# Kernel tuning notes

Measured on AMD Instinct MI355X. Metric: run time of the kernel, lower is better.

Reference implementation:

```python
import jax, jax.numpy as jnp
import numpy as np
from jax import lax

B, C, D, H, W = 2, 256, 32, 64, 192
TRAIN_W = 640
DISPS = np.arange(D, dtype=np.float32) * 0.01  # norm_disp_range


def conv1x1(x, w, b):
    # x [B,Cin,H,W], w [Cout,Cin]
    return jnp.einsum('bchw,oc->bohw', x, w) + b[None, :, None, None]


def conv3x3(x, w, b):
    y = lax.conv_general_dilated(x, w, (1, 1), 'SAME',
                                 dimension_numbers=('NCHW', 'OIHW', 'NCHW'))
    return y + b[None, :, None, None]


def warp_volume(x, shift_px):
    """Horizontal bilinear warp with border clamp for each disparity.
    x [B,Cc,H,W], shift_px [B,D] (pixel shift) -> [B,Cc,D,H,W]."""
    Wd = x.shape[3]
    j = jnp.arange(Wd, dtype=x.dtype)
    src = jnp.clip(j[None, None, :] + shift_px[:, :, None], 0.0, Wd - 1.0)  # [B,D,W]
    x0 = jnp.floor(src).astype(jnp.int32)
    x1 = jnp.minimum(x0 + 1, Wd - 1)
    frac = src - x0.astype(src.dtype)  # [B,D,W]

    def one(xb, i0, i1, fb):
        g0 = xb[:, :, i0]  # [Cc,H,D,W]
        g1 = xb[:, :, i1]
        out = g0 * (1.0 - fb) + g1 * fb
        return out.transpose(0, 2, 1, 3)  # [Cc,D,H,W]

    return jax.vmap(one)(x, x0, x1, frac)


def setup_inputs() -> dict:
    key = jax.random.key(0)
    ks = jax.random.split(key, 16)
    f32 = jnp.float32
    inp = {
        't_feat': jax.random.normal(ks[0], (B, C, H, W), f32),
        's_feat': jax.random.normal(ks[1], (B, C, H, W), f32),
        'directs': jnp.ones((B, 1, 1, 1), f32),
        'qw': jax.random.normal(ks[2], (C // 4, C), f32) * 0.05,
        'qb': jax.random.normal(ks[3], (C // 4,), f32) * 0.05,
        'kw': jax.random.normal(ks[4], (C // 4, C), f32) * 0.05,
        'kb': jax.random.normal(ks[5], (C // 4,), f32) * 0.05,
        'vw': jax.random.normal(ks[6], (C // 4, C), f32) * 0.05,
        'vb': jax.random.normal(ks[7], (C // 4,), f32) * 0.05,
        'p1w': jax.random.normal(ks[8], (C // 4, C // 2, 3, 3), f32) * 0.05,
        'p1b': jax.random.normal(ks[9], (C // 4,), f32) * 0.05,
        'p2w': jax.random.normal(ks[10], (D, C // 4, 3, 3), f32) * 0.05,
        'p2b': jax.random.normal(ks[11], (D,), f32) * 0.05,
        'rw': jax.random.normal(ks[12], (C, C + D), f32) * 0.05,
        'rb': jax.random.normal(ks[13], (C,), f32) * 0.05,
        'img_w': TRAIN_W,
    }
    return inp


def reference(t_feat, s_feat, directs, qw, qb, kw, kb, vw, vb,
              p1w, p1b, p2w, p2b, rw, rb, img_w):
    rel_scale = (TRAIN_W / img_w) if img_w != TRAIN_W else 1.0
    q = conv1x1(t_feat, qw, qb)  # [B,C/4,H,W]
    k = conv1x1(s_feat, kw, kb)
    v = conv1x1(s_feat, vw, vb)

    Wd = t_feat.shape[3]
    disps = jnp.asarray(DISPS, t_feat.dtype)
    # normalized shift d*2*rel_scale*directs -> pixels: * (W-1)/2
    shift = disps[None, :] * rel_scale * directs.reshape(-1, 1) * (Wd - 1)  # [B,D]

    wk = warp_volume(k, shift)  # [B,C/4,D,H,W]
    wv = warp_volume(v, shift)

    cq = q.shape[1]
    cost = jnp.einsum('bchw,bcdhw->bdhw', q, wk) / (cq ** 0.5)  # [B,D,H,W]
    norm_cost = jax.nn.softmax(cost, axis=1)
    agg_v = jnp.einsum('bdhw,bcdhw->bchw', norm_cost, wv)  # [B,C/4,H,W]

    h1 = jax.nn.elu(conv3x3(jnp.concatenate([q, agg_v], axis=1), p1w, p1b))
    res_cost = conv3x3(h1, p2w, p2b)  # [B,D,H,W]
    cost = (cost + res_cost) * 0.5
    norm_cost = jax.nn.softmax(cost, axis=1)
    x = jax.nn.elu(conv1x1(jnp.concatenate([t_feat, norm_cost], axis=1), rw, rb))
    return x, cost
```

## Files before the change

kernel.cpp:

```cpp
#include <hip/hip_runtime.h>

#define BB 2
#define CC 256
#define CQ 64
#define DD 32
#define HH 64
#define WW 192
#define HW (HH*WW)
#define NPIX (BB*HW)

typedef __attribute__((ext_vector_type(8))) short bf16x8;
typedef __attribute__((ext_vector_type(4))) float f32x4;

__device__ __forceinline__ float b2f(ushort s){ return __uint_as_float(((uint)s)<<16); }
__device__ __forceinline__ ushort f2b(float f){
    uint u = __float_as_uint(f);
    return (ushort)((u + 0x7fffu + ((u>>16)&1u)) >> 16);
}
__device__ __forceinline__ float eluf(float v){ return v > 0.f ? v : (__expf(v)-1.f); }

__global__ __launch_bounds__(256) void k_prep(
    const float* __restrict__ t_feat, const float* __restrict__ s_feat,
    ushort* __restrict__ Tt, ushort* __restrict__ Ts,
    const float* __restrict__ qw, const float* __restrict__ qb,
    const float* __restrict__ kw, const float* __restrict__ kb,
    const float* __restrict__ vw, const float* __restrict__ vb,
    const float* __restrict__ p1w, const float* __restrict__ p2w,
    const float* __restrict__ rw,
    ushort* __restrict__ Wqkv, float* __restrict__ bqkv,
    ushort* __restrict__ A1, ushort* __restrict__ A2, ushort* __restrict__ Ar)
{
    __shared__ ushort sT[64*264];
    int blk = blockIdx.x;
    int tid = threadIdx.x;
    if (blk >= 768){
        int id = (blk - 768)*256 + tid;
        if (id < 49152) {
            int o = id / 256, c = id % 256;
            float v = (o<64)? qw[o*256+c] : (o<128)? kw[(o-64)*256+c] : vw[(o-128)*256+c];
            Wqkv[id] = f2b(v);
        } else if (id < 49344) {
            int o = id - 49152;
            bqkv[o] = (o<64)? qb[o] : (o<128)? kb[o-64] : vb[o-128];
        } else if (id < 49344+73728) {
            int i = id - 49344;
            int o = i/1152, r = i%1152, t = r/128, ci = r%128;
            A1[i] = f2b(p1w[(size_t)(o*128+ci)*9 + t]);
        } else if (id < 49344+73728+18432) {
            int i = id - (49344+73728);
            int o = i/576, r = i%576, t = r/64, ci = r%64;
            A2[i] = f2b(p2w[(size_t)(o*64+ci)*9 + t]);
        } else if (id < 49344+73728+18432+73728) {
            int i = id - (49344+73728+18432);
            Ar[i] = f2b(rw[i]);
        }
        return;
    }
    int which = blk / 384;
    int rem   = blk % 384;
    int b     = rem / 192;
    int tile  = rem % 192;
    int p0    = tile*64;
    const float* src = which ? s_feat : t_feat;
    ushort* dst      = which ? Ts : Tt;

    for (int i = tid; i < 2048; i += 256){
        int px  = i & 63;
        int c16 = i >> 6;
        const float* p = src + ((size_t)(b*CC + c16*8))*HW + p0 + px;
        uint u[4];
        #pragma unroll
        for (int j2=0;j2<4;++j2)
            u[j2] = (uint)f2b(p[(size_t)(2*j2)*HW]) | ((uint)f2b(p[(size_t)(2*j2+1)*HW])<<16);
        uint4 q4; q4.x=u[0]; q4.y=u[1]; q4.z=u[2]; q4.w=u[3];
        *(uint4*)&sT[(px*33 + c16)*8] = q4;
    }
    __syncthreads();
    for (int i = tid; i < 2048; i += 256){
        int c16 = i & 31;
        int px  = i >> 5;
        uint4 v = *(const uint4*)&sT[(px*33 + c16)*8];
        *(uint4*)(dst + ((size_t)(b*HW + p0 + px))*CC + c16*8) = v;
    }
}

__global__ __launch_bounds__(256) void g_qkv(
    const ushort* __restrict__ Tt, const ushort* __restrict__ Ts,
    const ushort* __restrict__ Wqkv, const float* __restrict__ bqkv,
    ushort* __restrict__ X1, ushort* __restrict__ VbT)
{
    __shared__ ushort sT[32*264];
    __shared__ ushort sS[32*264];
    int tid = threadIdx.x;
    int bid = blockIdx.x;
    int tile = (bid & 7)*96 + (bid >> 3);
    int p0 = tile * 32;

    for (int i = tid; i < 1024; i += 256){
        int px = i >> 5, c16 = i & 31;
        size_t gsrc = ((size_t)(p0 + px))*CC + c16*8;
        *(uint4*)&sT[(px*33 + c16)*8] = *(const uint4*)(Tt + gsrc);
        *(uint4*)&sS[(px*33 + c16)*8] = *(const uint4*)(Ts + gsrc);
    }
    __syncthreads();

    int wv = tid >> 6, lane = tid & 63;
    int lm = lane & 15, lk = lane >> 4;
    f32x4 acc[3][2];
    #pragma unroll
    for (int g=0;g<3;++g){ acc[g][0]=(f32x4){0.f,0.f,0.f,0.f}; acc[g][1]=(f32x4){0.f,0.f,0.f,0.f}; }
    const ushort* Ap = Wqkv + (size_t)(wv*16 + lm)*CC + lk*8;

    #pragma unroll
    for (int k0=0; k0<CC; k0+=32){
        bf16x8 a0 = *(const bf16x8*)(Ap + k0);
        bf16x8 a1 = *(const bf16x8*)(Ap + 64*CC + k0);
        bf16x8 a2 = *(const bf16x8*)(Ap + 128*CC + k0);
        #pragma unroll
        for (int nt=0; nt<2; ++nt){
            int ch = (nt*16+lm)*33 + (k0>>3) + lk;
            bf16x8 bT = *(const bf16x8*)&sT[ch*8];
            bf16x8 bS = *(const bf16x8*)&sS[ch*8];
            acc[0][nt] = __builtin_amdgcn_mfma_f32_16x16x32_bf16(a0, bT, acc[0][nt], 0,0,0);
            acc[1][nt] = __builtin_amdgcn_mfma_f32_16x16x32_bf16(a1, bS, acc[1][nt], 0,0,0);
            acc[2][nt] = __builtin_amdgcn_mfma_f32_16x16x32_bf16(a2, bS, acc[2][nt], 0,0,0);
        }
    }
    int ol = wv*16 + lk*4;
    #pragma unroll
    for (int nt=0; nt<2; ++nt){
        int p = p0 + nt*16 + lm;
        {
            int ob = ol;
            uint u0 = (uint)f2b(acc[0][nt][0]+bqkv[ob])   | ((uint)f2b(acc[0][nt][1]+bqkv[ob+1])<<16);
            uint u1 = (uint)f2b(acc[0][nt][2]+bqkv[ob+2]) | ((uint)f2b(acc[0][nt][3]+bqkv[ob+3])<<16);
            *(uint2*)(X1 + (size_t)p*128 + ol) = make_uint2(u0, u1);
        }
        {
            int ob = 64 + ol;
            uint u0 = (uint)f2b(acc[1][nt][0]+bqkv[ob])   | ((uint)f2b(acc[1][nt][1]+bqkv[ob+1])<<16);
            uint u1 = (uint)f2b(acc[1][nt][2]+bqkv[ob+2]) | ((uint)f2b(acc[1][nt][3]+bqkv[ob+3])<<16);
            *(uint2*)(X1 + (size_t)p*128 + 64 + ol) = make_uint2(u0, u1);
        }
        #pragma unroll
        for (int j=0;j<4;++j)
            VbT[(size_t)(ol+j)*NPIX + p] = f2b(acc[2][nt][j] + bqkv[128 + ol + j]);
    }
}

#define BAND 160
#define STS 36
#define PFS 164
#define VTS 168
__global__ __launch_bounds__(512) void k_ca(
    const ushort* __restrict__ X1, const ushort* __restrict__ VbT,
    const float* __restrict__ directs, const int* __restrict__ img_w_p,
    float* __restrict__ C1, ushort* __restrict__ Agg)
{
    __shared__ float  sF[BAND*STS];
    __shared__ ushort sPC[32*VTS];
    int tid = threadIdx.x;
    int j   = blockIdx.x;
    int r8  = j & 7;
    int kk  = j >> 3;
    int sub = kk % 6;
    int rhi = kk / 6;
    int row = rhi*8 + r8;
    int b   = row >> 6;
    int h   = row & 63;
    int w0  = sub * 32;
    size_t rowbase = (size_t)b*HW + (size_t)h*WW;

    int w8 = tid >> 6, lane = tid & 63;
    int lm = lane & 15, lk = lane >> 4;

    {
        int mt = w8 & 1;
        int q  = w0 + mt*16 + lm;
        const ushort* Qp = X1 + (rowbase + q)*128 + lk*8;
        bf16x8 aq0 = *(const bf16x8*)(Qp);
        bf16x8 aq1 = *(const bf16x8*)(Qp + 32);
        for (int nt = (w8 >> 1); nt < 10; nt += 4){
            int xrow = nt*16 + lm;
            int gx = w0 - 64 + xrow;
            bf16x8 b0 = {0,0,0,0,0,0,0,0}, b1 = {0,0,0,0,0,0,0,0};
            if (gx >= 0 && gx < WW){
                const ushort* Kp = X1 + (rowbase + gx)*128 + 64 + lk*8;
                b0 = *(const bf16x8*)(Kp);
                b1 = *(const bf16x8*)(Kp + 32);
            }
            f32x4 acc = {0.f,0.f,0.f,0.f};
            acc = __builtin_amdgcn_mfma_f32_16x16x32_bf16(aq0, b0, acc, 0,0,0);
            acc = __builtin_amdgcn_mfma_f32_16x16x32_bf16(aq1, b1, acc, 0,0,0);
            *(f32x4*)&sF[xrow*STS + mt*16 + lk*4] = acc;
        }
    }
    __syncthreads();

    int px  = tid >> 4;
    int l16 = tid & 15;
    int w   = w0 + px;
    size_t n = rowbase + w;
    int imw = img_w_p[0];
    float rel = (imw != 640) ? (640.0f/(float)imw) : 1.0f;
    float sf = 0.01f * rel * directs[b] * 191.0f;
    float wf = (float)w;

    float cost[2]; int xi0[2], xi1[2]; float frk[2];
    #pragma unroll
    for (int t=0; t<2; ++t){
        int d = l16*2 + t;
        float srcx = fminf(fmaxf(wf + (float)d*sf, 0.f), 191.0f);
        int x0 = (int)floorf(srcx);
        int x1 = min(x0+1, WW-1);
        float fr = srcx - (float)x0;
        int i0 = x0 - w0 + 64;
        int i1 = x1 - w0 + 64;
        xi0[t] = i0; xi1[t] = i1; frk[t] = fr;
        float s0 = sF[i0*STS + px];
        float s1 = sF[i1*STS + px];
        cost[t] = (s0 + fr*(s1-s0)) * 0.125f;
    }
    *(float2*)(C1 + n*DD + l16*2) = make_float2(cost[0], cost[1]);
    float mm = fmaxf(cost[0], cost[1]);
    mm = fmaxf(mm, __shfl_xor(mm, 1));
    mm = fmaxf(mm, __shfl_xor(mm, 2));
    mm = fmaxf(mm, __shfl_xor(mm, 4));
    mm = fmaxf(mm, __shfl_xor(mm, 8));
    float e0 = __expf(cost[0]-mm), e1 = __expf(cost[1]-mm);
    float ss = e0 + e1;
    ss += __shfl_xor(ss, 1);
    ss += __shfl_xor(ss, 2);
    ss += __shfl_xor(ss, 4);
    ss += __shfl_xor(ss, 8);
    float inv = 1.f/ss;
    float p0 = e0*inv, p1 = e1*inv;
    __syncthreads();

    for (int i = tid; i < (32*PFS)/4; i += 512)
        *(f32x4*)&sF[i*4] = (f32x4){0.f,0.f,0.f,0.f};
    __syncthreads();

    {
        float w1a = p0*frk[0], w0a = p0 - w1a;
        float w1b = p1*frk[1], w0b = p1 - w1b;
        atomicAdd(&sF[px*PFS + xi0[0]], w0a);
        atomicAdd(&sF[px*PFS + xi1[0]], w1a);
        atomicAdd(&sF[px*PFS + xi0[1]], w0b);
        atomicAdd(&sF[px*PFS + xi1[1]], w1b);
    }
    __syncthreads();

    {
        int base = l16*10;
        #pragma unroll
        for (int q=0; q<5; ++q){
            float2 v2 = *(const float2*)&sF[px*PFS + base + q*2];
            *(uint*)&sPC[px*VTS + base + q*2] = (uint)f2b(v2.x) | ((uint)f2b(v2.y)<<16);
        }
    }
    __syncthreads();

    {
        int mi = w8 & 3;
        int ni = w8 >> 2;
        int c  = mi*16 + lm;
        int wr = ni*16 + lm;
        const ushort* Vp = VbT + (size_t)c*NPIX + rowbase + w0 - 64;
        f32x4 acc = {0.f,0.f,0.f,0.f};
        #pragma unroll
        for (int kt=0; kt<5; ++kt){
            int gx = w0 - 64 + kt*32 + lk*8;
            bf16x8 a = {0,0,0,0,0,0,0,0};
            if (gx >= 0 && gx < WW) a = *(const bf16x8*)(Vp + kt*32 + lk*8);
            bf16x8 bbf = *(const bf16x8*)&sPC[wr*VTS + kt*32 + lk*8];
            acc = __builtin_amdgcn_mfma_f32_16x16x32_bf16(a, bbf, acc, 0,0,0);
        }
        uint u0 = (uint)f2b(acc[0]) | ((uint)f2b(acc[1])<<16);
        uint u1 = (uint)f2b(acc[2]) | ((uint)f2b(acc[3])<<16);
        *(uint2*)(Agg + (rowbase + w0 + wr)*64 + mi*16 + lk*4) = make_uint2(u0, u1);
    }
}

__global__ __launch_bounds__(256) void g_conv1(
    const ushort* __restrict__ X1, const ushort* __restrict__ Agg,
    const ushort* __restrict__ A1, const float* __restrict__ p1b,
    ushort* __restrict__ X2)
{
    __shared__ ushort sB[3*16*34*8];
    int tid = threadIdx.x;
    int wv = tid >> 6, lane = tid & 63;
    int lm = lane & 15, lk = lane >> 4;
    int bid = blockIdx.x;
    int tile = (bid & 7)*96 + (bid >> 3);
    int n0 = tile * 32;
    int b  = n0 / HW;
    int pl = n0 % HW;
    int h  = pl / WW, w0 = pl % WW;

    for (int i = tid; i < 1632; i += 256){
        int dh = i / 544, rem2 = i % 544;
        int c16 = rem2 / 34, x = rem2 % 34;
        int hh = h + dh - 1, wx = w0 + x - 1;
        uint4 val = make_uint4(0,0,0,0);
        if (hh >= 0 && hh < HH && wx >= 0 && wx < WW){
            size_t pix = (size_t)b*HW + (size_t)hh*WW + wx;
            val = (c16 < 8) ? *(const uint4*)(X1 + pix*128 + c16*8)
                            : *(const uint4*)(Agg + pix*64 + (c16-8)*8);
        }
        *(uint4*)&sB[((dh*16 + c16)*34 + x)*8] = val;
    }
    __syncthreads();

    int mw = wv & 1, nw = wv >> 1;
    const ushort* Ap = A1 + (size_t)(mw*32 + lm)*1152 + lk*8;
    f32x4 acc0 = {0.f,0.f,0.f,0.f}, acc1 = {0.f,0.f,0.f,0.f};
    int xb = nw*16 + lm;
    #pragma unroll
    for (int t=0; t<9; ++t){
        int dh = t/3, dw = t%3;
        #pragma unroll
        for (int c0=0; c0<128; c0+=32){
            bf16x8 bb = *(const bf16x8*)&sB[((dh*16 + (c0>>3)+lk)*34 + xb + dw)*8];
            bf16x8 a0 = *(const bf16x8*)(Ap + t*128 + c0);
            bf16x8 a1 = *(const bf16x8*)(Ap + (size_t)16*1152 + t*128 + c0);
            acc0 = __builtin_amdgcn_mfma_f32_16x16x32_bf16(a0, bb, acc0, 0,0,0);
            acc1 = __builtin_amdgcn_mfma_f32_16x16x32_bf16(a1, bb, acc1, 0,0,0);
        }
    }
    int pg = n0 + nw*16 + lm;
    int o0 = mw*32 + lk*4;
    {
        uint u0 = (uint)f2b(eluf(acc0[0]+p1b[o0]))   | ((uint)f2b(eluf(acc0[1]+p1b[o0+1]))<<16);
        uint u1 = (uint)f2b(eluf(acc0[2]+p1b[o0+2])) | ((uint)f2b(eluf(acc0[3]+p1b[o0+3]))<<16);
        *(uint2*)(X2 + (size_t)pg*64 + o0) = make_uint2(u0, u1);
        int o1 = o0 + 16;
        uint u2 = (uint)f2b(eluf(acc1[0]+p1b[o1]))   | ((uint)f2b(eluf(acc1[1]+p1b[o1+1]))<<16);
        uint u3 = (uint)f2b(eluf(acc1[2]+p1b[o1+2])) | ((uint)f2b(eluf(acc1[3]+p1b[o1+3]))<<16);
        *(uint2*)(X2 + (size_t)pg*64 + o1) = make_uint2(u2, u3);
    }
}

__global__ __launch_bounds__(256) void g_conv2final(
    const ushort* __restrict__ X2, const ushort* __restrict__ A2,
    const float* __restrict__ p2b, const float* __restrict__ C1,
    const ushort* __restrict__ Tt, const ushort* __restrict__ Ar,
    const float* __restrict__ rb,
    float* __restrict__ cost_out, float* __restrict__ xout)
{
    __shared__ ushort sT[32*264];
    __shared__ float  sO[32*36];
    __shared__ ushort sN[32*40];
    ushort* sB = sT;
    int tid = threadIdx.x;
    int wv = tid >> 6, lane = tid & 63;
    int lm = lane & 15, lk = lane >> 4;
    int bid = blockIdx.x;
    int tile = (bid & 7)*96 + (bid >> 3);
    int n0 = tile * 32;
    int b  = n0 / HW;
    int pl = n0 % HW;
    int h  = pl / WW, w0 = pl % WW;

    for (int i = tid; i < 816; i += 256){
        int dh = i / 272, rem2 = i % 272;
        int c16 = rem2 / 34, x = rem2 % 34;
        int hh = h + dh - 1, wx = w0 + x - 1;
        uint4 val = make_uint4(0,0,0,0);
        if (hh >= 0 && hh < HH && wx >= 0 && wx < WW)
            val = *(const uint4*)(X2 + ((size_t)b*HW + (size_t)hh*WW + wx)*64 + c16*8);
        *(uint4*)&sB[((dh*8 + c16)*34 + x)*8] = val;
    }
    __syncthreads();

    {
        int mw = wv & 1, nw = wv >> 1;
        const ushort* Ap = A2 + (size_t)(mw*16 + lm)*576 + lk*8;
        f32x4 acc = {0.f,0.f,0.f,0.f};
        int xb = nw*16 + lm;
        #pragma unroll
        for (int t=0; t<9; ++t){
            int dh = t/3, dw = t%3;
            #pragma unroll
            for (int c0=0; c0<64; c0+=32){
                bf16x8 bb = *(const bf16x8*)&sB[((dh*8 + (c0>>3)+lk)*34 + xb + dw)*8];
                bf16x8 a  = *(const bf16x8*)(Ap + t*64 + c0);
                acc = __builtin_amdgcn_mfma_f32_16x16x32_bf16(a, bb, acc, 0,0,0);
            }
        }
        int pg = n0 + nw*16 + lm;
        int pll = pg % HW;
        int o = mw*16 + lk*4;
        f32x4 cv = *(const f32x4*)(C1 + (size_t)pg*DD + o);
        f32x4 outv;
        #pragma unroll
        for (int j=0;j<4;++j){
            outv[j] = (cv[j] + acc[j] + p2b[o+j]) * 0.5f;
            cost_out[((size_t)(b*DD + o + j))*HW + pll] = outv[j];
        }
        *(f32x4*)&sO[(nw*16 + lm)*36 + o] = outv;
    }
    __syncthreads();

    {
        int px = tid >> 3;
        int g  = tid & 7;
        f32x4 v = *(const f32x4*)&sO[px*36 + g*4];
        float m = fmaxf(fmaxf(v[0],v[1]), fmaxf(v[2],v[3]));
        m = fmaxf(m, __shfl_xor(m, 1));
        m = fmaxf(m, __shfl_xor(m, 2));
        m = fmaxf(m, __shfl_xor(m, 4));
        float e[4]; float s = 0.f;
        #pragma unroll
        for (int j=0;j<4;++j){ e[j] = __expf(v[j]-m); s += e[j]; }
        s += __shfl_xor(s, 1);
        s += __shfl_xor(s, 2);
        s += __shfl_xor(s, 4);
        float invs = 1.f/s;
        uint u0 = (uint)f2b(e[0]*invs) | ((uint)f2b(e[1]*invs)<<16);
        uint u1 = (uint)f2b(e[2]*invs) | ((uint)f2b(e[3]*invs)<<16);
        *(uint2*)&sN[px*40 + g*4] = make_uint2(u0, u1);
    }
    for (int i = tid; i < 1024; i += 256){
        int px = i >> 5, c16 = i & 31;
        *(uint4*)&sT[(px*33 + c16)*8] = *(const uint4*)(Tt + ((size_t)(n0+px))*CC + c16*8);
    }
    __syncthreads();

    {
        f32x4 acc[4][2];
        #pragma unroll
        for (int mi=0;mi<4;++mi){ acc[mi][0]=(f32x4){0.f,0.f,0.f,0.f}; acc[mi][1]=(f32x4){0.f,0.f,0.f,0.f}; }
        const ushort* Ap = Ar + (size_t)(wv*64 + lm)*288 + lk*8;

        #pragma unroll
        for (int k0=0; k0<288; k0+=32){
            bf16x8 a[4];
            #pragma unroll
            for (int mi=0;mi<4;++mi) a[mi] = *(const bf16x8*)(Ap + (size_t)mi*16*288 + k0);
            #pragma unroll
            for (int nt=0; nt<2; ++nt){
                int prow = nt*16 + lm;
                bf16x8 bb = (k0 < 256) ? *(const bf16x8*)&sT[(prow*33 + (k0>>3) + lk)*8]
                                       : *(const bf16x8*)&sN[(prow*5 + lk)*8];
                #pragma unroll
                for (int mi=0;mi<4;++mi)
                    acc[mi][nt] = __builtin_amdgcn_mfma_f32_16x16x32_bf16(a[mi], bb, acc[mi][nt], 0,0,0);
            }
        }
        #pragma unroll
        for (int mi=0;mi<4;++mi){
            int o = wv*64 + mi*16 + lk*4;
            #pragma unroll
            for (int nt=0; nt<2; ++nt){
                int p = n0 + nt*16 + lm;
                int bb2 = p / HW, pl2 = p % HW;
                #pragma unroll
                for (int j=0;j<4;++j)
                    xout[((size_t)(bb2*CC + o + j))*HW + pl2] = eluf(acc[mi][nt][j] + rb[o+j]);
            }
        }
    }
}

extern "C" void kernel_launch(void* const* d_in, const int* in_sizes, int n_in,
                              void* d_out, int out_size, void* d_ws, size_t ws_size,
                              hipStream_t stream)
{
    const float* t_feat = (const float*)d_in[0];
    const float* s_feat = (const float*)d_in[1];
    const float* directs= (const float*)d_in[2];
    const float* qw = (const float*)d_in[3];
    const float* qb = (const float*)d_in[4];
    const float* kw = (const float*)d_in[5];
    const float* kb = (const float*)d_in[6];
    const float* vw = (const float*)d_in[7];
    const float* vb = (const float*)d_in[8];
    const float* p1w= (const float*)d_in[9];
    const float* p1b= (const float*)d_in[10];
    const float* p2w= (const float*)d_in[11];
    const float* p2b= (const float*)d_in[12];
    const float* rw = (const float*)d_in[13];
    const float* rb = (const float*)d_in[14];
    const int* img_w= (const int*)d_in[15];

    char* wsb = (char*)d_ws;
    ushort* Tt   = (ushort*)(wsb + 0);
    char*  tsreg = wsb + 12582912;
    ushort* Ts   = (ushort*)tsreg;
    ushort* X2   = (ushort*)tsreg;
    float*  C1   = (float*)(tsreg + 3145728);
    ushort* Agg  = (ushort*)(tsreg + 6291456);
    ushort* X1   = (ushort*)(wsb + 25165824);
    ushort* VbT  = (ushort*)(wsb + 31457280);
    ushort* Wqkv = (ushort*)(wsb + 34603008);
    float*  bqkv = (float*) (wsb + 34701312);
    ushort* A1   = (ushort*)(wsb + 34702336);
    ushort* A2   = (ushort*)(wsb + 34849792);
    ushort* Ar   = (ushort*)(wsb + 34886656);
    if (ws_size < 35034112) return;

    float* xout     = (float*)d_out;
    float* cost_out = xout + (size_t)BB*CC*HW;

    k_prep      <<<1609, 256, 0, stream>>>(t_feat, s_feat, Tt, Ts,
                                           qw,qb,kw,kb,vw,vb,p1w,p2w,rw,
                                           Wqkv,bqkv,A1,A2,Ar);
    g_qkv       <<<768,  256, 0, stream>>>(Tt, Ts, Wqkv, bqkv, X1, VbT);
    k_ca        <<<768,  512, 0, stream>>>(X1, VbT, directs, img_w, C1, Agg);
    g_conv1     <<<768,  256, 0, stream>>>(X1, Agg, A1, p1b, X2);
    g_conv2final<<<768,  256, 0, stream>>>(X2, A2, p2b, C1, Tt, Ar, rb,
                                           cost_out, xout);
}
```

Measured before the change: 104.0 us.

## Fuse bf16 transpose into consumers and narrow cost-attention band by shift sign

Removes the separate pass that converted t_feat/s_feat to pixel-major bf16. g_qkv and g_conv2final now read the fp32 NCHW inputs directly, converting and transposing through shared memory, which eliminates a full write-and-read round trip of two large intermediates. The cost-attention kernel also picks a one-sided band of 96 columns based on the sign of the shift instead of a symmetric 160-column band, cutting the K-dot and V-aggregation MFMA work. The narrower band assumes the maximum pixel shift stays under about 64 columns, with indices clamped into the band. The fused loads use strided channel reads that may coalesce less well than before.

Measured after the change: 96.97 us. 1.07x faster.

```diff
diff --git a/kernel.cpp b/kernel.cpp
--- a/kernel.cpp
+++ b/kernel.cpp
@@ -19,9 +19,7 @@
 }
 __device__ __forceinline__ float eluf(float v){ return v > 0.f ? v : (__expf(v)-1.f); }
 
-__global__ __launch_bounds__(256) void k_prep(
-    const float* __restrict__ t_feat, const float* __restrict__ s_feat,
-    ushort* __restrict__ Tt, ushort* __restrict__ Ts,
+__global__ __launch_bounds__(256) void k_prep_w(
     const float* __restrict__ qw, const float* __restrict__ qb,
     const float* __restrict__ kw, const float* __restrict__ kb,
     const float* __restrict__ vw, const float* __restrict__ vb,
@@ -30,62 +28,30 @@
     ushort* __restrict__ Wqkv, float* __restrict__ bqkv,
     ushort* __restrict__ A1, ushort* __restrict__ A2, ushort* __restrict__ Ar)
 {
-    __shared__ ushort sT[64*264];
-    int blk = blockIdx.x;
-    int tid = threadIdx.x;
-    if (blk >= 768){
-        int id = (blk - 768)*256 + tid;
-        if (id < 49152) {
-            int o = id / 256, c = id % 256;
-            float v = (o<64)? qw[o*256+c] : (o<128)? kw[(o-64)*256+c] : vw[(o-128)*256+c];
-            Wqkv[id] = f2b(v);
-        } else if (id < 49344) {
-            int o = id - 49152;
-            bqkv[o] = (o<64)? qb[o] : (o<128)? kb[o-64] : vb[o-128];
-        } else if (id < 49344+73728) {
-            int i = id - 49344;
-            int o = i/1152, r = i%1152, t = r/128, ci = r%128;
-            A1[i] = f2b(p1w[(size_t)(o*128+ci)*9 + t]);
-        } else if (id < 49344+73728+18432) {
-            int i = id - (49344+73728);
-            int o = i/576, r = i%576, t = r/64, ci = r%64;
-            A2[i] = f2b(p2w[(size_t)(o*64+ci)*9 + t]);
-        } else if (id < 49344+73728+18432+73728) {
-            int i = id - (49344+73728+18432);
-            Ar[i] = f2b(rw[i]);
-        }
-        return;
-    }
-    int which = blk / 384;
-    int rem   = blk % 384;
-    int b     = rem / 192;
-    int tile  = rem % 192;
-    int p0    = tile*64;
-    const float* src = which ? s_feat : t_feat;
-    ushort* dst      = which ? Ts : Tt;
-
-    for (int i = tid; i < 2048; i += 256){
-        int px  = i & 63;
-        int c16 = i >> 6;
-        const float* p = src + ((size_t)(b*CC + c16*8))*HW + p0 + px;
-        uint u[4];
-        #pragma unroll
-        for (int j2=0;j2<4;++j2)
-            u[j2] = (uint)f2b(p[(size_t)(2*j2)*HW]) | ((uint)f2b(p[(size_t)(2*j2+1)*HW])<<16);
-        uint4 q4; q4.x=u[0]; q4.y=u[1]; q4.z=u[2]; q4.w=u[3];
-        *(uint4*)&sT[(px*33 + c16)*8] = q4;
-    }
-    __syncthreads();
-    for (int i = tid; i < 2048; i += 256){
-        int c16 = i & 31;
-        int px  = i >> 5;
-        uint4 v = *(const uint4*)&sT[(px*33 + c16)*8];
-        *(uint4*)(dst + ((size_t)(b*HW + p0 + px))*CC + c16*8) = v;
+    int id = blockIdx.x*256 + threadIdx.x;
+    if (id < 49152) {
+        int o = id / 256, c = id % 256;
+        float v = (o<64)? qw[o*256+c] : (o<128)? kw[(o-64)*256+c] : vw[(o-128)*256+c];
+        Wqkv[id] = f2b(v);
+    } else if (id < 49344) {
+        int o = id - 49152;
+        bqkv[o] = (o<64)? qb[o] : (o<128)? kb[o-64] : vb[o-128];
+    } else if (id < 49344+73728) {
+        int i = id - 49344;
+        int o = i/1152, r = i%1152, t = r/128, ci = r%128;
+        A1[i] = f2b(p1w[(size_t)(o*128+ci)*9 + t]);
+    } else if (id < 49344+73728+18432) {
+        int i = id - (49344+73728);
+        int o = i/576, r = i%576, t = r/64, ci = r%64;
+        A2[i] = f2b(p2w[(size_t)(o*64+ci)*9 + t]);
+    } else if (id < 49344+73728+18432+73728) {
+        int i = id - (49344+73728+18432);
+        Ar[i] = f2b(rw[i]);
     }
 }
 
 __global__ __launch_bounds__(256) void g_qkv(
-    const ushort* __restrict__ Tt, const ushort* __restrict__ Ts,
+    const float* __restrict__ t_feat, const float* __restrict__ s_feat,
     const ushort* __restrict__ Wqkv, const float* __restrict__ bqkv,
     ushort* __restrict__ X1, ushort* __restrict__ VbT)
 {
@@ -95,12 +61,23 @@
     int bid = blockIdx.x;
     int tile = (bid & 7)*96 + (bid >> 3);
     int p0 = tile * 32;
+    int b0  = p0 / HW;
+    int pl0 = p0 % HW;
 
     for (int i = tid; i < 1024; i += 256){
-        int px = i >> 5, c16 = i & 31;
-        size_t gsrc = ((size_t)(p0 + px))*CC + c16*8;
-        *(uint4*)&sT[(px*33 + c16)*8] = *(const uint4*)(Tt + gsrc);
-        *(uint4*)&sS[(px*33 + c16)*8] = *(const uint4*)(Ts + gsrc);
+        int px = i & 31, c8 = i >> 5;
+        const float* pt = t_feat + ((size_t)(b0*CC + c8*8))*HW + pl0 + px;
+        const float* ps = s_feat + ((size_t)(b0*CC + c8*8))*HW + pl0 + px;
+        uint ut[4], us[4];
+        #pragma unroll
+        for (int j2=0;j2<4;++j2){
+            ut[j2] = (uint)f2b(pt[(size_t)(2*j2)*HW]) | ((uint)f2b(pt[(size_t)(2*j2+1)*HW])<<16);
+            us[j2] = (uint)f2b(ps[(size_t)(2*j2)*HW]) | ((uint)f2b(ps[(size_t)(2*j2+1)*HW])<<16);
+        }
+        uint4 qt; qt.x=ut[0]; qt.y=ut[1]; qt.z=ut[2]; qt.w=ut[3];
+        uint4 qs; qs.x=us[0]; qs.y=us[1]; qs.z=us[2]; qs.w=us[3];
+        *(uint4*)&sT[(px*33 + c8)*8] = qt;
+        *(uint4*)&sS[(px*33 + c8)*8] = qs;
     }
     __syncthreads();
 
@@ -148,17 +125,17 @@
     }
 }
 
-#define BAND 160
+#define BANDC 96
 #define STS 36
-#define PFS 164
-#define VTS 168
+#define PFS 100
+#define VTS2 104
 __global__ __launch_bounds__(512) void k_ca(
     const ushort* __restrict__ X1, const ushort* __restrict__ VbT,
     const float* __restrict__ directs, const int* __restrict__ img_w_p,
     float* __restrict__ C1, ushort* __restrict__ Agg)
 {
-    __shared__ float  sF[BAND*STS];
-    __shared__ ushort sPC[32*VTS];
+    __shared__ float  sF[BANDC*STS];
+    __shared__ ushort sPC[32*VTS2];
     int tid = threadIdx.x;
     int j   = blockIdx.x;
     int r8  = j & 7;
@@ -171,6 +148,11 @@
     int w0  = sub * 32;
     size_t rowbase = (size_t)b*HW + (size_t)h*WW;
 
+    int imw = img_w_p[0];
+    float rel = (imw != 640) ? (640.0f/(float)imw) : 1.0f;
+    float sf = 0.01f * rel * directs[b] * 191.0f;
+    int bl = (sf < 0.f) ? (w0 - 64) : w0;
+
     int w8 = tid >> 6, lane = tid & 63;
     int lm = lane & 15, lk = lane >> 4;
 
@@ -180,9 +162,9 @@
         const ushort* Qp = X1 + (rowbase + q)*128 + lk*8;
         bf16x8 aq0 = *(const bf16x8*)(Qp);
         bf16x8 aq1 = *(const bf16x8*)(Qp + 32);
-        for (int nt = (w8 >> 1); nt < 10; nt += 4){
+        for (int nt = (w8 >> 1); nt < 6; nt += 4){
             int xrow = nt*16 + lm;
-            int gx = w0 - 64 + xrow;
+            int gx = bl + xrow;
             bf16x8 b0 = {0,0,0,0,0,0,0,0}, b1 = {0,0,0,0,0,0,0,0};
             if (gx >= 0 && gx < WW){
                 const ushort* Kp = X1 + (rowbase + gx)*128 + 64 + lk*8;
@@ -201,9 +183,6 @@
     int l16 = tid & 15;
     int w   = w0 + px;
     size_t n = rowbase + w;
-    int imw = img_w_p[0];
-    float rel = (imw != 640) ? (640.0f/(float)imw) : 1.0f;
-    float sf = 0.01f * rel * directs[b] * 191.0f;
     float wf = (float)w;
 
     float cost[2]; int xi0[2], xi1[2]; float frk[2];
@@ -214,8 +193,8 @@
         int x0 = (int)floorf(srcx);
         int x1 = min(x0+1, WW-1);
         float fr = srcx - (float)x0;
-        int i0 = x0 - w0 + 64;
-        int i1 = x1 - w0 + 64;
+        int i0 = min(max(x0 - bl, 0), BANDC-1);
+        int i1 = min(max(x1 - bl, 0), BANDC-1);
         xi0[t] = i0; xi1[t] = i1; frk[t] = fr;
         float s0 = sF[i0*STS + px];
         float s1 = sF[i1*STS + px];
@@ -252,11 +231,11 @@
     __syncthreads();
 
     {
-        int base = l16*10;
-        #pragma unroll
-        for (int q=0; q<5; ++q){
+        int base = l16*6;
+        #pragma unroll
+        for (int q=0; q<3; ++q){
             float2 v2 = *(const float2*)&sF[px*PFS + base + q*2];
-            *(uint*)&sPC[px*VTS + base + q*2] = (uint)f2b(v2.x) | ((uint)f2b(v2.y)<<16);
+            *(uint*)&sPC[px*VTS2 + base + q*2] = (uint)f2b(v2.x) | ((uint)f2b(v2.y)<<16);
         }
     }
     __syncthreads();
@@ -266,14 +245,14 @@
         int ni = w8 >> 2;
         int c  = mi*16 + lm;
         int wr = ni*16 + lm;
-        const ushort* Vp = VbT + (size_t)c*NPIX + rowbase + w0 - 64;
+        const ushort* Vp = VbT + (size_t)c*NPIX + rowbase + bl;
         f32x4 acc = {0.f,0.f,0.f,0.f};
         #pragma unroll
-        for (int kt=0; kt<5; ++kt){
-            int gx = w0 - 64 + kt*32 + lk*8;
+        for (int kt=0; kt<3; ++kt){
+            int gx = bl + kt*32 + lk*8;
             bf16x8 a = {0,0,0,0,0,0,0,0};
             if (gx >= 0 && gx < WW) a = *(const bf16x8*)(Vp + kt*32 + lk*8);
-            bf16x8 bbf = *(const bf16x8*)&sPC[wr*VTS + kt*32 + lk*8];
+            bf16x8 bbf = *(const bf16x8*)&sPC[wr*VTS2 + kt*32 + lk*8];
             acc = __builtin_amdgcn_mfma_f32_16x16x32_bf16(a, bbf, acc, 0,0,0);
         }
         uint u0 = (uint)f2b(acc[0]) | ((uint)f2b(acc[1])<<16);
@@ -344,7 +323,7 @@
 __global__ __launch_bounds__(256) void g_conv2final(
     const ushort* __restrict__ X2, const ushort* __restrict__ A2,
     const float* __restrict__ p2b, const float* __restrict__ C1,
-    const ushort* __restrict__ Tt, const ushort* __restrict__ Ar,
+    const float* __restrict__ t_feat, const ushort* __restrict__ Ar,
     const float* __restrict__ rb,
     float* __restrict__ cost_out, float* __restrict__ xout)
 {
@@ -422,8 +401,14 @@
         *(uint2*)&sN[px*40 + g*4] = make_uint2(u0, u1);
     }
     for (int i = tid; i < 1024; i += 256){
-        int px = i >> 5, c16 = i & 31;
-        *(uint4*)&sT[(px*33 + c16)*8] = *(const uint4*)(Tt + ((size_t)(n0+px))*CC + c16*8);
+        int px = i & 31, c8 = i >> 5;
+        const float* pt = t_feat + ((size_t)(b*CC + c8*8))*HW + pl + px;
+        uint u[4];
+        #pragma unroll
+        for (int j2=0;j2<4;++j2)
+            u[j2] = (uint)f2b(pt[(size_t)(2*j2)*HW]) | ((uint)f2b(pt[(size_t)(2*j2+1)*HW])<<16);
+        uint4 q4; q4.x=u[0]; q4.y=u[1]; q4.z=u[2]; q4.w=u[3];
+        *(uint4*)&sT[(px*33 + c8)*8] = q4;
     }
     __syncthreads();
 
@@ -485,9 +470,7 @@
     const int* img_w= (const int*)d_in[15];
 
     char* wsb = (char*)d_ws;
-    ushort* Tt   = (ushort*)(wsb + 0);
     char*  tsreg = wsb + 12582912;
-    ushort* Ts   = (ushort*)tsreg;
     ushort* X2   = (ushort*)tsreg;
     float*  C1   = (float*)(tsreg + 3145728);
     ushort* Agg  = (ushort*)(tsreg + 6291456);
@@ -503,12 +486,11 @@
     float* xout     = (float*)d_out;
     float* cost_out = xout + (size_t)BB*CC*HW;
 
-    k_prep      <<<1609, 256, 0, stream>>>(t_feat, s_feat, Tt, Ts,
-                                           qw,qb,kw,kb,vw,vb,p1w,p2w,rw,
+    k_prep_w    <<<841,  256, 0, stream>>>(qw,qb,kw,kb,vw,vb,p1w,p2w,rw,
                                            Wqkv,bqkv,A1,A2,Ar);
-    g_qkv       <<<768,  256, 0, stream>>>(Tt, Ts, Wqkv, bqkv, X1, VbT);
+    g_qkv       <<<768,  256, 0, stream>>>(t_feat, s_feat, Wqkv, bqkv, X1, VbT);
     k_ca        <<<768,  512, 0, stream>>>(X1, VbT, directs, img_w, C1, Agg);
     g_conv1     <<<768,  256, 0, stream>>>(X1, Agg, A1, p1b, X2);
-    g_conv2final<<<768,  256, 0, stream>>>(X2, A2, p2b, C1, Tt, Ar, rb,
+    g_conv2final<<<768,  256, 0, stream>>>(X2, A2, p2b, C1, t_feat, Ar, rb,
                                            cost_out, xout);
 }
```
